# Optimization experiments

Measured on AMD Instinct MI355X. Metric: run time of the kernel, lower is better.

## Reference

```python
import jax, jax.numpy as jnp
import numpy as np


def setup_inputs() -> dict:
    key = jax.random.key(0)
    k0, k1, k2, k3 = jax.random.split(key, 4)
    B, in_dim, n_vars, out_dim, E = 64, 512, 512, 720, 8
    x = jax.random.normal(k0, (B, in_dim, n_vars), dtype=jnp.float32)
    # Gating: nn.Linear(in_dim, E, bias=False) -> weight [E, in_dim]
    Wg = jax.random.normal(k1, (E, in_dim), dtype=jnp.float32) * 0.02
    # Experts: nn.Linear(in_dim, out_dim) -> weight [out_dim, in_dim], bias [out_dim]
    We = jax.random.normal(k2, (E, out_dim, in_dim), dtype=jnp.float32) * 0.02
    be = jax.random.normal(k3, (E, out_dim), dtype=jnp.float32) * 0.02
    return {"x": x, "Wg": Wg, "We": We, "be": be, "top_k": 2}


def reference(x, Wg, We, be, top_k):
    # x: [B, in_len, n_vars] -> tokens along n_vars with feature dim in_len
    xt = jnp.swapaxes(x, 1, 2)                      # [B, V, D]
    gate = jax.nn.softmax(xt @ Wg.T, axis=-1)       # [B, V, E]
    weights, sel = jax.lax.top_k(gate, top_k)       # [B, V, k]
    E, O, D = We.shape
    out = jnp.zeros(xt.shape[:2] + (O,), dtype=xt.dtype)  # [B, V, O]
    for e in range(E):
        # combine weight for expert e: sum over top-k slots routed to e
        coef = jnp.sum(jnp.where(sel == e, weights, jnp.zeros_like(weights)), axis=-1)  # [B, V]
        out = out + coef[..., None] * (jnp.einsum('bvd,od->bvo', xt, We[e]) + be[e])
    return jnp.swapaxes(out, 1, 2)                  # [B, pred_len, n_vars]
```

## Files before the change

### kernel.cpp

```cpp
#include <hip/hip_runtime.h>
#include <hip/hip_bf16.h>

#define DID 512
#define NV  512
#define NB  64
#define OD  720
#define OPAD 768
#define NE  8
#define NTOK (NB * NV)
#define MAXTILE 512

typedef short  bf16x8 __attribute__((ext_vector_type(8)));
typedef float  f32x4  __attribute__((ext_vector_type(4)));

#define XT_OFF    0u
#define WB_OFF    33554432u
#define PID_OFF   39845888u
#define C1D_OFF   39976960u
#define C2D_OFF   40108032u
#define TL_OFF    40239104u
#define CL1_OFF   40370176u
#define CL2_OFF   40501248u
#define BCNT_OFF  40632320u
#define BFILL_OFF 40632576u
#define BOFF_OFF  40632832u
#define TPID_OFF  40633088u
#define TT0_OFF   40635136u
#define TEND_OFF  40637184u
#define NT_OFF    40639232u
#define SCR_OFF   40639488u
#define SCR_END   87825408u

static __device__ __forceinline__ ushort f2bf(float f) {
  unsigned u = __float_as_uint(f);
  unsigned r = (u + 0x7fffu + ((u >> 16) & 1u)) >> 16;
  return (ushort)r;
}
static __device__ __forceinline__ float bf2f(ushort u) {
  return __uint_as_float(((unsigned)u) << 16);
}
static __device__ __forceinline__ void async16(const ushort* g, ushort* l) {
  __builtin_amdgcn_global_load_lds((__attribute__((address_space(1))) void*)(g),
                                   (__attribute__((address_space(3))) void*)(l),
                                   16, 0, 0);
}
static __device__ __forceinline__ int swz(int r) { return (r & 3) ^ ((r >> 2) & 1); }

__global__ __launch_bounds__(512) void k_gatet(const float* __restrict__ x,
                                               const float* __restrict__ Wg,
                                               ushort* __restrict__ xt,
                                               int* __restrict__ pairid,
                                               float* __restrict__ c1d,
                                               float* __restrict__ c2d,
                                               int* __restrict__ bcnt) {
  __shared__ float wg[NE * DID];
  __shared__ float part[8][64][NE + 1];
  __shared__ int cnt64[64];
  const int tid = threadIdx.x;
  for (int i = tid; i < NE * DID / 4; i += 512)
    ((float4*)wg)[i] = ((const float4*)Wg)[i];
  if (tid < 64) cnt64[tid] = 0;
  __syncthreads();

  const int b    = blockIdx.y;
  const int v0   = blockIdx.x * 64;
  const int w    = tid >> 6;
  const int lane = tid & 63;
  const int v    = v0 + lane;
  const int d0   = w * 64;
  const float* xp = x + ((size_t)b * DID + d0) * NV + v;
  ushort* xtp = xt + ((size_t)b * NV + v) * DID + d0;

  float acc[NE];
#pragma unroll
  for (int e = 0; e < NE; ++e) acc[e] = 0.f;

  for (int c = 0; c < 64; c += 8) {
    float xv[8];
#pragma unroll
    for (int u = 0; u < 8; ++u) xv[u] = xp[(size_t)(c + u) * NV];
#pragma unroll
    for (int e = 0; e < NE; ++e) {
      const float* wp = &wg[e * DID + d0 + c];
      float4 wa = *(const float4*)wp;
      float4 wb4 = *(const float4*)(wp + 4);
      acc[e] += xv[0] * wa.x + xv[1] * wa.y + xv[2] * wa.z + xv[3] * wa.w
              + xv[4] * wb4.x + xv[5] * wb4.y + xv[6] * wb4.z + xv[7] * wb4.w;
    }
    bf16x8 pk;
#pragma unroll
    for (int u = 0; u < 8; ++u) pk[u] = (short)f2bf(xv[u]);
    *(bf16x8*)(xtp + c) = pk;
  }

#pragma unroll
  for (int e = 0; e < NE; ++e) part[w][lane][e] = acc[e];
  __syncthreads();

  if (tid < 64) {
    float a[NE];
#pragma unroll
    for (int e = 0; e < NE; ++e) {
      float s = part[0][tid][e];
#pragma unroll
      for (int q = 1; q < 8; ++q) s += part[q][tid][e];
      a[e] = s;
    }
    float mx = a[0];
#pragma unroll
    for (int e = 1; e < NE; ++e) mx = fmaxf(mx, a[e]);
    float sum = 0.f;
#pragma unroll
    for (int e = 0; e < NE; ++e) { a[e] = __expf(a[e] - mx); sum += a[e]; }
    const float inv = 1.f / sum;

    int i1 = 0; float g1 = a[0];
#pragma unroll
    for (int e = 1; e < NE; ++e) if (a[e] > g1) { g1 = a[e]; i1 = e; }
    int i2 = -1; float g2 = -1.f;
#pragma unroll
    for (int e = 0; e < NE; ++e) if (e != i1 && a[e] > g2) { g2 = a[e]; i2 = e; }
    g1 *= inv; g2 *= inv;

    int ea, eb; float ca, cb;
    if (i1 < i2) { ea = i1; eb = i2; ca = g1; cb = g2; }
    else         { ea = i2; eb = i1; ca = g2; cb = g1; }
    const int pid = ea * 8 + eb;
    const int t = b * NV + v0 + tid;
    pairid[t] = pid; c1d[t] = ca; c2d[t] = cb;
    atomicAdd(&cnt64[pid], 1);
  }
  __syncthreads();
  if (tid < 64 && cnt64[tid]) atomicAdd(&bcnt[tid], cnt64[tid]);
}

__global__ __launch_bounds__(256) void k_wbconv(const float* __restrict__ We,
                                                ushort* __restrict__ wb) {
  const int e = blockIdx.y;
  const int i = blockIdx.x * 256 + threadIdx.x;
  const int o = i >> 9;
  ushort val = 0;
  if (o < OD) val = f2bf(We[(size_t)e * OD * DID + i]);
  wb[(size_t)e * OPAD * DID + i] = val;
}

__global__ void k_prefix(const int* __restrict__ bcnt, int* __restrict__ boffs,
                         int* __restrict__ tpid, int* __restrict__ tt0,
                         int* __restrict__ tend, int* __restrict__ ntp) {
  const int p = threadIdx.x;
  const int c = bcnt[p];
  int run = c;
#pragma unroll
  for (int s = 1; s < 64; s <<= 1) {
    int up = __shfl_up(run, s, 64);
    if (p >= s) run += up;
  }
  const int excl = run - c;
  boffs[p] = excl;
  const int ntiles = (c + 127) >> 7;
  int trun = ntiles;
#pragma unroll
  for (int s = 1; s < 64; s <<= 1) {
    int up = __shfl_up(trun, s, 64);
    if (p >= s) trun += up;
  }
  const int texcl = trun - ntiles;
  for (int i = 0; i < ntiles; ++i) {
    tpid[texcl + i] = p;
    tt0[texcl + i]  = excl + i * 128;
    tend[texcl + i] = excl + c;
  }
  if (p == 63) ntp[0] = texcl + ntiles;
}

__global__ __launch_bounds__(256) void k_scatter(const int* __restrict__ pairid,
                                                 const float* __restrict__ c1d,
                                                 const float* __restrict__ c2d,
                                                 const int* __restrict__ boffs,
                                                 int* __restrict__ bfill,
                                                 int* __restrict__ tlist,
                                                 float* __restrict__ cl1,
                                                 float* __restrict__ cl2) {
  __shared__ int cnt64[64], base64[64];
  const int tid = threadIdx.x;
  if (tid < 64) cnt64[tid] = 0;
  __syncthreads();
  const int t = blockIdx.x * 256 + tid;
  const int pid = pairid[t];
  const int p = atomicAdd(&cnt64[pid], 1);
  __syncthreads();
  if (tid < 64) base64[tid] = cnt64[tid] ? atomicAdd(&bfill[tid], cnt64[tid]) : 0;
  __syncthreads();
  const int slot = boffs[pid] + base64[pid] + p;
  tlist[slot] = t; cl1[slot] = c1d[t]; cl2[slot] = c2d[t];
}

__global__ __launch_bounds__(256, 2) void k_gemm(
    const ushort* __restrict__ xt, const ushort* __restrict__ wb,
    const float* __restrict__ be, const int* __restrict__ tlist,
    const float* __restrict__ cl1, const float* __restrict__ cl2,
    const int* __restrict__ tpid, const int* __restrict__ tt0,
    const int* __restrict__ tendarr, const int* __restrict__ ntp,
    ushort* __restrict__ scratch, float* __restrict__ out, int mode) {
  const int tile = blockIdx.x;
  if (tile >= ntp[0]) return;
  const int pid  = tpid[tile];
  const int t0   = tt0[tile];
  const int tend = tendarr[tile];
  const int e1 = pid >> 3, e2 = pid & 7;
  const int o0 = blockIdx.y * 128;

  __shared__ __align__(16) ushort As[2][4096];
  __shared__ __align__(16) ushort Bs[2][4096];

  const int tid  = threadIdx.x;
  const int lane = tid & 63;
  const int w    = tid >> 6;

  const int f0 = w * 128 + lane, f1 = f0 + 64;
  const int r0 = f0 >> 2, p0 = f0 & 3, q0 = p0 ^ swz(r0);
  const int r1 = f1 >> 2, p1 = f1 & 3, q1 = p1 ^ swz(r1);

  const int aoff0 = (o0 + r0) * DID + q0 * 8;
  const int aoff1 = (o0 + r1) * DID + q1 * 8;
  const int sl0 = t0 + r0, sl1 = t0 + r1;
  const int tok0 = (sl0 < tend) ? tlist[sl0] : 0;
  const int tok1 = (sl1 < tend) ? tlist[sl1] : 0;
  const int boff0 = tok0 * DID + q0 * 8;
  const int boff1 = tok1 * DID + q1 * 8;
  const int dA0 = w * 1024, dA1 = w * 1024 + 512;

  const int m    = lane & 15;
  const int quad = lane >> 4;
  const int wo   = (w >> 1) * 64;
  const int wt   = (w & 1) * 64;

  f32x4 acc[4][4];
#pragma unroll
  for (int i = 0; i < 4; ++i)
#pragma unroll
    for (int j = 0; j < 4; ++j) acc[i][j] = (f32x4){0.f, 0.f, 0.f, 0.f};

  {
    const ushort* wA = wb + (size_t)e1 * OPAD * DID;
    async16(wA + aoff0, &As[0][dA0]);
    async16(wA + aoff1, &As[0][dA1]);
    async16(xt + boff0, &Bs[0][dA0]);
    async16(xt + boff1, &Bs[0][dA1]);
  }

  for (int kk = 0; kk < 32; ++kk) {
    __syncthreads();

    if (kk == 16) {
      float ratio[4];
#pragma unroll
      for (int j = 0; j < 4; ++j) {
        const int sl = t0 + wt + j * 16 + m;
        const bool g = sl < tend;
        const float cc1 = g ? cl1[sl] : 0.f;
        const float cc2 = g ? cl2[sl] : 1.f;
        ratio[j] = cc1 / cc2;
      }
      const float* be1p = be + e1 * OD;
#pragma unroll
      for (int i = 0; i < 4; ++i) {
        const int ob = o0 + wo + i * 16 + quad * 4;
        float b0 = 0, b1 = 0, b2 = 0, b3 = 0;
        if (ob < OD) { b0 = be1p[ob]; b1 = be1p[ob + 1]; b2 = be1p[ob + 2]; b3 = be1p[ob + 3]; }
#pragma unroll
        for (int j = 0; j < 4; ++j) {
          acc[i][j][0] = (acc[i][j][0] + b0) * ratio[j];
          acc[i][j][1] = (acc[i][j][1] + b1) * ratio[j];
          acc[i][j][2] = (acc[i][j][2] + b2) * ratio[j];
          acc[i][j][3] = (acc[i][j][3] + b3) * ratio[j];
        }
      }
    }

    const int nk = kk + 1;
    if (nk < 32) {
      const int nb = nk & 1;
      const int eA = (nk < 16) ? e1 : e2;
      const int k0 = (nk & 15) * 32;
      const ushort* wA = wb + (size_t)eA * OPAD * DID + k0;
      async16(wA + aoff0, &As[nb][dA0]);
      async16(wA + aoff1, &As[nb][dA1]);
      async16(xt + boff0 + k0, &Bs[nb][dA0]);
      async16(xt + boff1 + k0, &Bs[nb][dA1]);
    }

    const int cb = kk & 1;
    bf16x8 af[4], bfr[4];
#pragma unroll
    for (int i = 0; i < 4; ++i) {
      const int R = wo + i * 16 + m;
      af[i] = *(const bf16x8*)(&As[cb][R * 32 + ((quad ^ swz(R)) << 3)]);
    }
#pragma unroll
    for (int j = 0; j < 4; ++j) {
      const int R = wt + j * 16 + m;
      bfr[j] = *(const bf16x8*)(&Bs[cb][R * 32 + ((quad ^ swz(R)) << 3)]);
    }
#pragma unroll
    for (int i = 0; i < 4; ++i)
#pragma unroll
      for (int j = 0; j < 4; ++j)
        acc[i][j] = __builtin_amdgcn_mfma_f32_16x16x32_bf16(af[i], bfr[j],
                                                            acc[i][j], 0, 0, 0);
  }

  float c2v[4]; int tokv[4]; bool gv[4];
#pragma unroll
  for (int j = 0; j < 4; ++j) {
    const int sl = t0 + wt + j * 16 + m;
    gv[j] = sl < tend;
    c2v[j]  = gv[j] ? cl2[sl] : 0.f;
    tokv[j] = gv[j] ? tlist[sl] : 0;
  }
  const float* be2p = be + e2 * OD;
#pragma unroll
  for (int i = 0; i < 4; ++i) {
    const int ob = o0 + wo + i * 16 + quad * 4;
    if (ob < OD) {
      const float b0 = be2p[ob], b1 = be2p[ob + 1], b2 = be2p[ob + 2], b3 = be2p[ob + 3];
#pragma unroll
      for (int j = 0; j < 4; ++j) {
        if (gv[j]) {
          const float v0 = c2v[j] * (acc[i][j][0] + b0);
          const float v1 = c2v[j] * (acc[i][j][1] + b1);
          const float v2 = c2v[j] * (acc[i][j][2] + b2);
          const float v3 = c2v[j] * (acc[i][j][3] + b3);
          if (mode == 0) {
            ushort4 pk = make_ushort4(f2bf(v0), f2bf(v1), f2bf(v2), f2bf(v3));
            *(ushort4*)(scratch + (size_t)tokv[j] * OD + ob) = pk;
          } else {
            const int bb = tokv[j] >> 9, vv = tokv[j] & 511;
            float* op = out + ((size_t)bb * OD + ob) * NV + vv;
            op[0] = v0; op[(size_t)NV] = v1; op[2 * (size_t)NV] = v2; op[3 * (size_t)NV] = v3;
          }
        }
      }
    }
  }
}

__global__ __launch_bounds__(256) void k_combine(const ushort* __restrict__ scratch,
                                                 float* __restrict__ out) {
  __shared__ ushort s[64][68];
  const int v0 = blockIdx.x * 64;
  const int o0 = blockIdx.y * 64;
  const int b  = blockIdx.z;
  const int tid = threadIdx.x;
#pragma unroll
  for (int it = 0; it < 2; ++it) {
    const int c = it * 256 + tid;
    const int row = c >> 3, cg = c & 7;
    const int o = o0 + cg * 8;
    if (o + 8 <= OD) {
      const ushort* src = scratch + ((size_t)(b * NV + v0 + row)) * OD + o;
      ushort4 ua = *(const ushort4*)(src);
      ushort4 ub = *(const ushort4*)(src + 4);
      *(ushort4*)&s[row][cg * 8] = ua;
      *(ushort4*)&s[row][cg * 8 + 4] = ub;
    }
  }
  __syncthreads();
  const int vv = tid & 63;
  const int og = tid >> 6;
#pragma unroll
  for (int oi = 0; oi < 8; ++oi) {
    const int ol = (og * 8 + oi) * 2;
    const int o = o0 + ol;
    if (o < OD) {
      ushort2 u = *(const ushort2*)&s[vv][ol];
      float* op = out + ((size_t)b * OD + o) * NV + v0 + vv;
      op[0]  = bf2f(u.x);
      op[NV] = bf2f(u.y);
    }
  }
}

extern "C" void kernel_launch(void* const* d_in, const int* in_sizes, int n_in,
                              void* d_out, int out_size, void* d_ws, size_t ws_size,
                              hipStream_t stream) {
  const float* x  = (const float*)d_in[0];
  const float* Wg = (const float*)d_in[1];
  const float* We = (const float*)d_in[2];
  const float* be = (const float*)d_in[3];
  float* out = (float*)d_out;

  char* ws = (char*)d_ws;
  ushort* xt     = (ushort*)(ws + XT_OFF);
  ushort* wb     = (ushort*)(ws + WB_OFF);
  int*    pairid = (int*)   (ws + PID_OFF);
  float*  c1d    = (float*) (ws + C1D_OFF);
  float*  c2d    = (float*) (ws + C2D_OFF);
  int*    tlist  = (int*)   (ws + TL_OFF);
  float*  cl1    = (float*) (ws + CL1_OFF);
  float*  cl2    = (float*) (ws + CL2_OFF);
  int*    bcnt   = (int*)   (ws + BCNT_OFF);
  int*    bfill  = (int*)   (ws + BFILL_OFF);
  int*    boffs  = (int*)   (ws + BOFF_OFF);
  int*    tpid   = (int*)   (ws + TPID_OFF);
  int*    tt0    = (int*)   (ws + TT0_OFF);
  int*    tend   = (int*)   (ws + TEND_OFF);
  int*    ntp    = (int*)   (ws + NT_OFF);
  ushort* scratch= (ushort*)(ws + SCR_OFF);

  const int mode = (ws_size >= (size_t)SCR_END) ? 0 : 1;

  (void)hipMemsetAsync(bcnt, 0, 512, stream);

  k_gatet<<<dim3(NV / 64, NB), 512, 0, stream>>>(x, Wg, xt, pairid, c1d, c2d, bcnt);
  k_wbconv<<<dim3(OPAD * DID / 256, NE), 256, 0, stream>>>(We, wb);
  k_prefix<<<1, 64, 0, stream>>>(bcnt, boffs, tpid, tt0, tend, ntp);
  k_scatter<<<NTOK / 256, 256, 0, stream>>>(pairid, c1d, c2d, boffs, bfill,
                                            tlist, cl1, cl2);
  k_gemm<<<dim3(320, OPAD / 128), 256, 0, stream>>>(xt, wb, be, tlist, cl1, cl2,
                                                    tpid, tt0, tend, ntp,
                                                    scratch, out, mode);
  if (mode == 0)
    k_combine<<<dim3(NV / 64, (OD + 63) / 64, NB), 256, 0, stream>>>(scratch, out);
}
```

Measured before the change: 322.1 us.

## Triple-buffer GEMM K-loop with explicit waitcnt and MFMA priority boost

Replaces the double-buffered LDS pipeline in the expert GEMM with a three-stage ring that keeps two tiles of loads in flight. Each step uses a manual s_waitcnt vmcnt plus s_barrier, and the last three steps are peeled into a drain epilogue. The MFMA block is wrapped in s_setprio, and the per-token coefficient and token-index loads are hoisted before the loop. This aims to hide global-load latency better, at the cost of 50% more shared memory per block and fragile hand-written wait counts that assume each stage issues exactly four loads.

```diff
diff --git a/kernel.cpp b/kernel.cpp
--- a/kernel.cpp
+++ b/kernel.cpp
@@ -210,8 +210,8 @@
   const int e1 = pid >> 3, e2 = pid & 7;
   const int o0 = blockIdx.y * 128;
 
-  __shared__ __align__(16) ushort As[2][4096];
-  __shared__ __align__(16) ushort Bs[2][4096];
+  __shared__ __align__(16) ushort As[3][4096];
+  __shared__ __align__(16) ushort Bs[3][4096];
 
   const int tid  = threadIdx.x;
   const int lane = tid & 63;
@@ -235,33 +235,71 @@
   const int wo   = (w >> 1) * 64;
   const int wt   = (w & 1) * 64;
 
+  float ratio[4], c2v[4]; int tokv[4]; bool gv[4];
+#pragma unroll
+  for (int j = 0; j < 4; ++j) {
+    const int sl = t0 + wt + j * 16 + m;
+    gv[j] = sl < tend;
+    const float cc1 = gv[j] ? cl1[sl] : 0.f;
+    const float cc2 = gv[j] ? cl2[sl] : 1.f;
+    ratio[j] = cc1 / cc2;
+    c2v[j]   = gv[j] ? cc2 : 0.f;
+    tokv[j]  = gv[j] ? tlist[sl] : 0;
+  }
+
   f32x4 acc[4][4];
 #pragma unroll
   for (int i = 0; i < 4; ++i)
 #pragma unroll
     for (int j = 0; j < 4; ++j) acc[i][j] = (f32x4){0.f, 0.f, 0.f, 0.f};
 
-  {
-    const ushort* wA = wb + (size_t)e1 * OPAD * DID;
-    async16(wA + aoff0, &As[0][dA0]);
-    async16(wA + aoff1, &As[0][dA1]);
-    async16(xt + boff0, &Bs[0][dA0]);
-    async16(xt + boff1, &Bs[0][dA1]);
-  }
-
-  for (int kk = 0; kk < 32; ++kk) {
-    __syncthreads();
+#define STAGE(t, buf) do {                                          \
+    const int eA_ = ((t) < 16) ? e1 : e2;                           \
+    const int k0_ = ((t) & 15) * 32;                                \
+    const ushort* wA_ = wb + (size_t)eA_ * OPAD * DID + k0_;        \
+    async16(wA_ + aoff0, &As[buf][dA0]);                            \
+    async16(wA_ + aoff1, &As[buf][dA1]);                            \
+    async16(xt + boff0 + k0_, &Bs[buf][dA0]);                       \
+    async16(xt + boff1 + k0_, &Bs[buf][dA1]);                       \
+  } while (0)
+
+#define FRAGS(buf)                                                       \
+    bf16x8 af[4], bfr[4];                                                \
+    {                                                                    \
+      const ushort* Asb = &As[buf][0];                                   \
+      const ushort* Bsb = &Bs[buf][0];                                   \
+      _Pragma("unroll")                                                  \
+      for (int i = 0; i < 4; ++i) {                                      \
+        const int R = wo + i * 16 + m;                                   \
+        af[i] = *(const bf16x8*)(Asb + R * 32 + ((quad ^ swz(R)) << 3)); \
+      }                                                                  \
+      _Pragma("unroll")                                                  \
+      for (int j = 0; j < 4; ++j) {                                      \
+        const int R = wt + j * 16 + m;                                   \
+        bfr[j] = *(const bf16x8*)(Bsb + R * 32 + ((quad ^ swz(R)) << 3));\
+      }                                                                  \
+    }
+
+#define MFMA16()                                                         \
+    __builtin_amdgcn_s_setprio(1);                                       \
+    _Pragma("unroll")                                                    \
+    for (int i = 0; i < 4; ++i)                                          \
+      _Pragma("unroll")                                                  \
+      for (int j = 0; j < 4; ++j)                                        \
+        acc[i][j] = __builtin_amdgcn_mfma_f32_16x16x32_bf16(af[i], bfr[j],\
+                                                            acc[i][j], 0, 0, 0); \
+    __builtin_amdgcn_s_setprio(0);
+
+  STAGE(0, 0);
+  STAGE(1, 1);
+  STAGE(2, 2);
+
+  int cur = 0;
+  for (int kk = 0; kk < 29; ++kk) {
+    asm volatile("s_waitcnt vmcnt(8)" ::: "memory");
+    __builtin_amdgcn_s_barrier();
 
     if (kk == 16) {
-      float ratio[4];
-#pragma unroll
-      for (int j = 0; j < 4; ++j) {
-        const int sl = t0 + wt + j * 16 + m;
-        const bool g = sl < tend;
-        const float cc1 = g ? cl1[sl] : 0.f;
-        const float cc2 = g ? cl2[sl] : 1.f;
-        ratio[j] = cc1 / cc2;
-      }
       const float* be1p = be + e1 * OD;
 #pragma unroll
       for (int i = 0; i < 4; ++i) {
@@ -278,46 +316,37 @@
       }
     }
 
-    const int nk = kk + 1;
-    if (nk < 32) {
-      const int nb = nk & 1;
-      const int eA = (nk < 16) ? e1 : e2;
-      const int k0 = (nk & 15) * 32;
-      const ushort* wA = wb + (size_t)eA * OPAD * DID + k0;
-      async16(wA + aoff0, &As[nb][dA0]);
-      async16(wA + aoff1, &As[nb][dA1]);
-      async16(xt + boff0 + k0, &Bs[nb][dA0]);
-      async16(xt + boff1 + k0, &Bs[nb][dA1]);
-    }
-
-    const int cb = kk & 1;
-    bf16x8 af[4], bfr[4];
-#pragma unroll
-    for (int i = 0; i < 4; ++i) {
-      const int R = wo + i * 16 + m;
-      af[i] = *(const bf16x8*)(&As[cb][R * 32 + ((quad ^ swz(R)) << 3)]);
-    }
-#pragma unroll
-    for (int j = 0; j < 4; ++j) {
-      const int R = wt + j * 16 + m;
-      bfr[j] = *(const bf16x8*)(&Bs[cb][R * 32 + ((quad ^ swz(R)) << 3)]);
-    }
-#pragma unroll
-    for (int i = 0; i < 4; ++i)
-#pragma unroll
-      for (int j = 0; j < 4; ++j)
-        acc[i][j] = __builtin_amdgcn_mfma_f32_16x16x32_bf16(af[i], bfr[j],
-                                                            acc[i][j], 0, 0, 0);
-  }
-
-  float c2v[4]; int tokv[4]; bool gv[4];
-#pragma unroll
-  for (int j = 0; j < 4; ++j) {
-    const int sl = t0 + wt + j * 16 + m;
-    gv[j] = sl < tend;
-    c2v[j]  = gv[j] ? cl2[sl] : 0.f;
-    tokv[j] = gv[j] ? tlist[sl] : 0;
-  }
+    FRAGS(cur)
+    asm volatile("s_waitcnt lgkmcnt(0)" ::: "memory");
+    __builtin_amdgcn_s_barrier();
+    STAGE(kk + 3, cur);
+    MFMA16()
+    cur = (cur == 2) ? 0 : cur + 1;
+  }
+
+  {
+    asm volatile("s_waitcnt vmcnt(8)" ::: "memory");
+    __builtin_amdgcn_s_barrier();
+    FRAGS(2)
+    MFMA16()
+  }
+  {
+    asm volatile("s_waitcnt vmcnt(4)" ::: "memory");
+    __builtin_amdgcn_s_barrier();
+    FRAGS(0)
+    MFMA16()
+  }
+  {
+    asm volatile("s_waitcnt vmcnt(0)" ::: "memory");
+    __builtin_amdgcn_s_barrier();
+    FRAGS(1)
+    MFMA16()
+  }
+
+#undef STAGE
+#undef FRAGS
+#undef MFMA16
+
   const float* be2p = be + e2 * OD;
 #pragma unroll
   for (int i = 0; i < 4; ++i) {
```

New measurement: 324.2 us. About the same (+0.6%).
